# Kernel tuning notes

Hardware: AMD Instinct MI355X
Metric: run time of the kernel (lower is better)

## Reference

```python
import jax, jax.numpy as jnp
import numpy as np

E = 256  # embed_dim (hardcoded in source module)
H = 4    # n_head
D = E // H
SEQ = 32768


def setup_inputs() -> dict:
    key = jax.random.key(0)
    ks = jax.random.split(key, 5)
    x = jax.random.normal(ks[0], (SEQ, E), dtype=jnp.float32)
    in_proj_weight = jax.random.normal(ks[1], (3 * E, E), dtype=jnp.float32) * (1.0 / np.sqrt(E))
    in_proj_bias = jax.random.normal(ks[2], (3 * E,), dtype=jnp.float32) * 0.02
    out_proj_weight = jax.random.normal(ks[3], (E, E), dtype=jnp.float32) * (1.0 / np.sqrt(E))
    out_proj_bias = jax.random.normal(ks[4], (E,), dtype=jnp.float32) * 0.02
    return {
        "x": x,
        "in_proj_weight": in_proj_weight,
        "in_proj_bias": in_proj_bias,
        "out_proj_weight": out_proj_weight,
        "out_proj_bias": out_proj_bias,
    }


def reference(x, in_proj_weight, in_proj_bias, out_proj_weight, out_proj_bias):
    # QKV projections (q uses only the first token of x: single-query decode attention)
    Wq, Wk, Wv = in_proj_weight[:E], in_proj_weight[E:2 * E], in_proj_weight[2 * E:]
    bq, bk, bv = in_proj_bias[:E], in_proj_bias[E:2 * E], in_proj_bias[2 * E:]
    q = x[:1] @ Wq.T + bq            # [1, E]
    k = x @ Wk.T + bk                # [S, E]
    v = x @ Wv.T + bv                # [S, E]

    qh = q.reshape(H, D)             # [H, D] (single query)
    kh = k.reshape(-1, H, D)         # [S, H, D]
    vh = v.reshape(-1, H, D)         # [S, H, D]

    scale = 1.0 / np.sqrt(D).astype(np.float32)
    scores = jnp.einsum("hd,shd->hs", qh, kh) * scale   # [H, S]
    attn = jax.nn.softmax(scores, axis=-1)                # [H, S]
    ctx = jnp.einsum("hs,shd->hd", attn, vh)             # [H, D]

    out = ctx.reshape(1, E) @ out_proj_weight.T + out_proj_bias  # [1, E]
    return out
```

## Files before the change

kernel.cpp:

```cpp
#include <hip/hip_runtime.h>
#include <hip/hip_cooperative_groups.h>
namespace cg = cooperative_groups;

#define NBLK 256
#define WS_LP   0
#define WS_YV   1024
#define WS_B2   2048
#define WS_KQ   2304
#define WS_C4   3328
#define WS_M2   3392
#define WS_YP   265536

__device__ __forceinline__ float dot4(float4 a, float4 b) {
  return a.x * b.x + a.y * b.y + a.z * b.z + a.w * b.w;
}

__device__ __forceinline__ void phaseA_kq(const float* __restrict__ x, const float* __restrict__ W,
                                          const float* __restrict__ inb, float* __restrict__ kq,
                                          float* __restrict__ c4, float* sh, int bid, int t) {
  float* xs = sh;
  float* qls = sh + 256;
  float* red = sh + 320;
  const int lane = t & 63, w = t >> 6;
  const int h = bid >> 2, qt = bid & 3;
  if (t < 256) xs[t] = x[t];
  __syncthreads();
  const float4 xv = *(const float4*)&xs[lane * 4];
#pragma unroll
  for (int k = 0; k < 8; ++k) {
    const int eloc = w * 8 + k;
    const int row = h * 64 + eloc;
    float4 wv = *(const float4*)&W[(size_t)row * 256 + lane * 4];
    float p = dot4(wv, xv);
#pragma unroll
    for (int m = 1; m < 64; m <<= 1) p += __shfl_xor(p, m);
    if (lane == 0) qls[eloc] = p + inb[row];
  }
  __syncthreads();
  const int cl = t & 63, ds = t >> 6;
  float acc = 0.f;
#pragma unroll
  for (int d2 = 0; d2 < 8; ++d2) {
    const int d = ds * 8 + d2;
    acc += W[(size_t)(256 + h * 64 + d) * 256 + qt * 64 + cl] * qls[d];
  }
  red[ds * 64 + cl] = acc;
  __syncthreads();
  if (ds == 0) {
    float s = 0.f;
#pragma unroll
    for (int i = 0; i < 8; ++i) s += red[i * 64 + cl];
    kq[h * 256 + qt * 64 + cl] = s;
  }
  if (qt == 0 && t < 64) {
    float v = qls[t] * inb[256 + h * 64 + t];
#pragma unroll
    for (int m = 1; m < 64; m <<= 1) v += __shfl_xor(v, m);
    if (t == 0) c4[h] = v;
  }
}

__device__ __forceinline__ void phaseA_m2(const float* __restrict__ W, const float* __restrict__ Wout,
                                          float* __restrict__ M2, float* sh, int b2, int t) {
  float* wout_t = sh;
  const int tile = b2 >> 1, sub = b2 & 1;
  const int h = tile >> 4, e0 = (tile & 15) * 16 + sub * 8;
  {
    const int e = t >> 6, d = t & 63;
    wout_t[e * 64 + d] = Wout[(size_t)(e0 + e) * 256 + h * 64 + d];
  }
  __syncthreads();
  const int c = t & 255, eh = t >> 8;
  float acc[4] = {0.f, 0.f, 0.f, 0.f};
#pragma unroll 8
  for (int d = 0; d < 64; ++d) {
    const float wv = W[(size_t)(512 + h * 64 + d) * 256 + c];
#pragma unroll
    for (int e = 0; e < 4; ++e) acc[e] += wv * wout_t[(eh * 4 + e) * 64 + d];
  }
#pragma unroll
  for (int e = 0; e < 4; ++e)
    M2[(size_t)(e0 + eh * 4 + e) * 1024 + h * 256 + c] = acc[e];
}

__device__ __forceinline__ void phaseA_b2(const float* __restrict__ Wout, const float* __restrict__ inb,
                                          const float* __restrict__ bout, float* __restrict__ bias2,
                                          float* sh, int b, int t) {
  float* red = sh;
  const int og = t >> 5, seg = t & 31;
  const int e = b * 16 + og;
  float acc = 0.f;
#pragma unroll
  for (int j = 0; j < 8; ++j)
    acc += Wout[(size_t)e * 256 + seg * 8 + j] * inb[512 + seg * 8 + j];
  red[og * 32 + seg] = acc;
  __syncthreads();
  if (t < 16) {
    float s = bout[b * 16 + t];
#pragma unroll
    for (int i = 0; i < 32; ++i) s += red[t * 32 + i];
    bias2[b * 16 + t] = s;
  }
}

__device__ __forceinline__ float bscore(float4 xv, float4 kq0, float4 kq1, float4 kq2,
                                        float4 kq3, float c4v, int lane) {
  float p0 = dot4(xv, kq0), p1 = dot4(xv, kq1), p2 = dot4(xv, kq2), p3 = dot4(xv, kq3);
  const bool b1 = (lane & 2) != 0;
  float keep0 = b1 ? p2 : p0, send0 = b1 ? p0 : p2;
  keep0 += __shfl_xor(send0, 2);
  float keep1 = b1 ? p3 : p1, send1 = b1 ? p1 : p3;
  keep1 += __shfl_xor(send1, 2);
  const bool b0 = (lane & 1) != 0;
  float vv = b0 ? keep1 : keep0, sv = b0 ? keep0 : keep1;
  vv += __shfl_xor(sv, 1);
  vv += __shfl_xor(vv, 4);
  vv += __shfl_xor(vv, 8);
  vv += __shfl_xor(vv, 16);
  vv += __shfl_xor(vv, 32);
  return (vv + c4v) * 0.125f;
}

__device__ __forceinline__ void phaseB_core(const float4* xvA, const float4* xvB,
                                            const float* __restrict__ kq, const float* __restrict__ c4,
                                            float* __restrict__ ypart, float* __restrict__ lpart,
                                            float* yls, int bid, int t) {
  float* sll = yls + 8192;
  const int lane = t & 63, w = t >> 6;
  const int hme = lane & 3;
  const float4 kq0 = *(const float4*)&kq[0 * 256 + lane * 4];
  const float4 kq1 = *(const float4*)&kq[1 * 256 + lane * 4];
  const float4 kq2 = *(const float4*)&kq[2 * 256 + lane * 4];
  const float4 kq3 = *(const float4*)&kq[3 * 256 + lane * 4];
  const float c4v = c4[hme];

  float vA[8], vB[8];
#pragma unroll
  for (int r = 0; r < 8; ++r) vA[r] = bscore(xvA[r], kq0, kq1, kq2, kq3, c4v, lane);
#pragma unroll
  for (int r = 0; r < 8; ++r) vB[r] = bscore(xvB[r], kq0, kq1, kq2, kq3, c4v, lane);

  float l = 0.f;
  float4 a[4];
#pragma unroll
  for (int k = 0; k < 4; ++k) a[k] = (float4){0.f, 0.f, 0.f, 0.f};
#pragma unroll
  for (int r = 0; r < 8; ++r) {
    const float e0 = __expf(vA[r]);
    l += e0;
    const float e1 = __shfl_xor(e0, 1);
    const float e2 = __shfl_xor(e0, 2);
    const float e3 = __shfl_xor(e0, 3);
    a[0].x += e0 * xvA[r].x; a[0].y += e0 * xvA[r].y; a[0].z += e0 * xvA[r].z; a[0].w += e0 * xvA[r].w;
    a[1].x += e1 * xvA[r].x; a[1].y += e1 * xvA[r].y; a[1].z += e1 * xvA[r].z; a[1].w += e1 * xvA[r].w;
    a[2].x += e2 * xvA[r].x; a[2].y += e2 * xvA[r].y; a[2].z += e2 * xvA[r].z; a[2].w += e2 * xvA[r].w;
    a[3].x += e3 * xvA[r].x; a[3].y += e3 * xvA[r].y; a[3].z += e3 * xvA[r].z; a[3].w += e3 * xvA[r].w;
  }
#pragma unroll
  for (int r = 0; r < 8; ++r) {
    const float e0 = __expf(vB[r]);
    l += e0;
    const float e1 = __shfl_xor(e0, 1);
    const float e2 = __shfl_xor(e0, 2);
    const float e3 = __shfl_xor(e0, 3);
    a[0].x += e0 * xvB[r].x; a[0].y += e0 * xvB[r].y; a[0].z += e0 * xvB[r].z; a[0].w += e0 * xvB[r].w;
    a[1].x += e1 * xvB[r].x; a[1].y += e1 * xvB[r].y; a[1].z += e1 * xvB[r].z; a[1].w += e1 * xvB[r].w;
    a[2].x += e2 * xvB[r].x; a[2].y += e2 * xvB[r].y; a[2].z += e2 * xvB[r].z; a[2].w += e2 * xvB[r].w;
    a[3].x += e3 * xvB[r].x; a[3].y += e3 * xvB[r].y; a[3].z += e3 * xvB[r].z; a[3].w += e3 * xvB[r].w;
  }

  __syncthreads();
  if (lane < 4) sll[w * 4 + lane] = l;
#pragma unroll
  for (int k = 0; k < 4; ++k) {
    const int h = hme ^ k;
    *(float4*)&yls[w * 1024 + h * 256 + lane * 4] = a[k];
  }
  __syncthreads();

  if (t < 4) {
    float lb = 0.f;
#pragma unroll
    for (int i = 0; i < 8; ++i) lb += sll[i * 4 + t];
    lpart[t * NBLK + bid] = lb;
  }
  float* yp = &ypart[(size_t)bid * 1024];
#pragma unroll
  for (int o = t; o < 1024; o += 512) {
    float s = 0.f;
#pragma unroll
    for (int i = 0; i < 8; ++i) s += yls[i * 1024 + o];
    yp[o] = s;
  }
}

__device__ __forceinline__ void phaseC(const float* __restrict__ ypart, const float* __restrict__ lpart,
                                       float* __restrict__ z, float* sh, int bid, int t) {
  float* lred = sh;
  float* sred = sh + 256;
  const int h = bid >> 4;
  const int o0 = bid * 16;
  if (t < 256) lred[t] = lpart[h * 256 + t];
  __syncthreads();
  for (int s = 128; s > 0; s >>= 1) {
    if (t < s) lred[t] += lred[t + s];
    __syncthreads();
  }
  const float inv = 1.0f / lred[0];
  const int ol = t & 15, bg = t >> 4;
  float s = 0.f;
#pragma unroll
  for (int j = 0; j < 8; ++j) {
    const int b = bg * 8 + j;
    s += ypart[(size_t)b * 1024 + o0 + ol];
  }
  sred[bg * 16 + ol] = s;
  __syncthreads();
  if (t < 16) {
    float tot = 0.f;
#pragma unroll
    for (int g = 0; g < 32; ++g) tot += sred[g * 16 + t];
    z[o0 + t] = tot * inv;
  }
}

__device__ __forceinline__ void phaseD(const float* __restrict__ M2, const float* __restrict__ z,
                                       const float* __restrict__ bias2, float* __restrict__ out,
                                       float* sh, int bid, int t) {
  float* zls = sh;
  float* smo = sh + 1024;
  for (int i = t; i < 1024; i += 512) zls[i] = z[i];
  __syncthreads();
  const int og = t >> 5, seg = t & 31;
  const int e = bid * 16 + og;
  float acc = 0.f;
  const float4* m4 = (const float4*)&M2[(size_t)e * 1024 + seg * 32];
  const float4* z4 = (const float4*)&zls[seg * 32];
#pragma unroll
  for (int j = 0; j < 8; ++j) acc += dot4(m4[j], z4[j]);
  smo[og * 32 + seg] = acc;
  __syncthreads();
  if (t < 16) {
    float s = bias2[bid * 16 + t];
#pragma unroll
    for (int i = 0; i < 32; ++i) s += smo[t * 32 + i];
    out[bid * 16 + t] = s;
  }
}

__global__ void __launch_bounds__(512, 1) mha_coop(const float* __restrict__ x,
                                                   const float* __restrict__ W,
                                                   const float* __restrict__ inb,
                                                   const float* __restrict__ Wout,
                                                   const float* __restrict__ bout,
                                                   float* __restrict__ out,
                                                   float* __restrict__ ws) {
  __shared__ __align__(16) float sh[8224];
  const int t = threadIdx.x, bid = blockIdx.x;
  const int lane = t & 63, w = t >> 6;
  cg::grid_group grid = cg::this_grid();

  const int r0 = bid * 128 + w * 16;
  float4 xvA[8], xvB[8];

  if (bid >= 16) {
#pragma unroll
    for (int r = 0; r < 8; ++r)
      xvA[r] = *(const float4*)&x[(size_t)(r0 + r) * 256 + lane * 4];
#pragma unroll
    for (int r = 0; r < 8; ++r)
      xvB[r] = *(const float4*)&x[(size_t)(r0 + 8 + r) * 256 + lane * 4];
  }

  if (bid < 16) {
    phaseA_kq(x, W, inb, ws + WS_KQ, ws + WS_C4, sh, bid, t);
#pragma unroll
    for (int r = 0; r < 8; ++r)
      xvA[r] = *(const float4*)&x[(size_t)(r0 + r) * 256 + lane * 4];
#pragma unroll
    for (int r = 0; r < 8; ++r)
      xvB[r] = *(const float4*)&x[(size_t)(r0 + 8 + r) * 256 + lane * 4];
  } else if (bid < 144) {
    phaseA_m2(W, Wout, ws + WS_M2, sh, bid - 16, t);
  } else if (bid < 160) {
    phaseA_b2(Wout, inb, bout, ws + WS_B2, sh, bid - 144, t);
  }

  grid.sync();
  phaseB_core(xvA, xvB, ws + WS_KQ, ws + WS_C4, ws + WS_YP, ws + WS_LP, sh, bid, t);
  grid.sync();
  if (bid < 64) phaseC(ws + WS_YP, ws + WS_LP, ws + WS_YV, sh, bid, t);
  grid.sync();
  if (bid < 16) phaseD(ws + WS_M2, ws + WS_YV, ws + WS_B2, out, sh, bid, t);
}

__global__ void __launch_bounds__(512) fb_A(const float* __restrict__ x, const float* __restrict__ W,
                                            const float* __restrict__ inb, const float* __restrict__ Wout,
                                            const float* __restrict__ bout, float* __restrict__ ws) {
  __shared__ __align__(16) float sh[832];
  const int bid = blockIdx.x, t = threadIdx.x;
  if (bid < 16) phaseA_kq(x, W, inb, ws + WS_KQ, ws + WS_C4, sh, bid, t);
  else if (bid < 144) phaseA_m2(W, Wout, ws + WS_M2, sh, bid - 16, t);
  else if (bid < 160) phaseA_b2(Wout, inb, bout, ws + WS_B2, sh, bid - 144, t);
}
__global__ void __launch_bounds__(512) fb_B(const float* __restrict__ x, float* __restrict__ ws) {
  __shared__ __align__(16) float sh[8224];
  const int bid = blockIdx.x, t = threadIdx.x;
  const int lane = t & 63, w = t >> 6;
  const int r0 = bid * 128 + w * 16;
  float4 xvA[8], xvB[8];
#pragma unroll
  for (int r = 0; r < 8; ++r)
    xvA[r] = *(const float4*)&x[(size_t)(r0 + r) * 256 + lane * 4];
#pragma unroll
  for (int r = 0; r < 8; ++r)
    xvB[r] = *(const float4*)&x[(size_t)(r0 + 8 + r) * 256 + lane * 4];
  phaseB_core(xvA, xvB, ws + WS_KQ, ws + WS_C4, ws + WS_YP, ws + WS_LP, sh, bid, t);
}
__global__ void __launch_bounds__(512) fb_C(float* __restrict__ ws) {
  __shared__ __align__(16) float sh[768];
  phaseC(ws + WS_YP, ws + WS_LP, ws + WS_YV, sh, blockIdx.x, threadIdx.x);
}
__global__ void __launch_bounds__(512) fb_D(float* __restrict__ out, float* __restrict__ ws) {
  __shared__ __align__(16) float sh[1536];
  phaseD(ws + WS_M2, ws + WS_YV, ws + WS_B2, out, sh, blockIdx.x, threadIdx.x);
}

extern "C" void kernel_launch(void* const* d_in, const int* in_sizes, int n_in,
                              void* d_out, int out_size, void* d_ws, size_t ws_size,
                              hipStream_t stream) {
  const float* x = (const float*)d_in[0];
  const float* W = (const float*)d_in[1];
  const float* inb = (const float*)d_in[2];
  const float* Wout = (const float*)d_in[3];
  const float* bout = (const float*)d_in[4];
  float* out = (float*)d_out;
  float* ws = (float*)d_ws;

  int dev = 0;
  (void)hipGetDevice(&dev);
  int coopAttr = 0, ncu = 0, occ = 0;
  bool coop = (hipDeviceGetAttribute(&coopAttr, hipDeviceAttributeCooperativeLaunch, dev) == hipSuccess) &&
              coopAttr != 0;
  coop = coop &&
         (hipDeviceGetAttribute(&ncu, hipDeviceAttributeMultiprocessorCount, dev) == hipSuccess);
  coop = coop &&
         (hipOccupancyMaxActiveBlocksPerMultiprocessor(&occ, mha_coop, 512, 0) == hipSuccess);
  coop = coop && (occ * ncu >= NBLK);

  if (coop) {
    void* args[] = {(void*)&x, (void*)&W, (void*)&inb, (void*)&Wout,
                    (void*)&bout, (void*)&out, (void*)&ws};
    if (hipLaunchCooperativeKernel((const void*)mha_coop, dim3(NBLK), dim3(512),
                                   args, 0, stream) == hipSuccess)
      return;
  }
  fb_A<<<160, 512, 0, stream>>>(x, W, inb, Wout, bout, ws);
  fb_B<<<NBLK, 512, 0, stream>>>(x, ws);
  fb_C<<<64, 512, 0, stream>>>(ws);
  fb_D<<<16, 512, 0, stream>>>(out, ws);
}
```

Before: 31.87 us.

## Project per-block context through Wv in phase B and drop M2 precompute

Removes the precomputed M2 = Wv^T·Wout fusion and bias2 blocks. Each phase-B block now multiplies its partial x-weighted sums by Wv to produce a 256-wide per-block context partial. A single final phase reduces the partials, normalises by the softmax sums, adds the value bias and applies the output projection. This removes one grid-wide sync and the large M2 matrix write and read, at the cost of every block reading the full 256x256 Wv slice.

```diff
diff --git a/kernel.cpp b/kernel.cpp
--- a/kernel.cpp
+++ b/kernel.cpp
@@ -4,12 +4,9 @@
 
 #define NBLK 256
 #define WS_LP   0
-#define WS_YV   1024
-#define WS_B2   2048
-#define WS_KQ   2304
-#define WS_C4   3328
-#define WS_M2   3392
-#define WS_YP   265536
+#define WS_KQ   1024
+#define WS_C4   2048
+#define WS_CTXP 2112
 
 __device__ __forceinline__ float dot4(float4 a, float4 b) {
   return a.x * b.x + a.y * b.y + a.z * b.z + a.w * b.w;
@@ -57,49 +54,6 @@
 #pragma unroll
     for (int m = 1; m < 64; m <<= 1) v += __shfl_xor(v, m);
     if (t == 0) c4[h] = v;
-  }
-}
-
-__device__ __forceinline__ void phaseA_m2(const float* __restrict__ W, const float* __restrict__ Wout,
-                                          float* __restrict__ M2, float* sh, int b2, int t) {
-  float* wout_t = sh;
-  const int tile = b2 >> 1, sub = b2 & 1;
-  const int h = tile >> 4, e0 = (tile & 15) * 16 + sub * 8;
-  {
-    const int e = t >> 6, d = t & 63;
-    wout_t[e * 64 + d] = Wout[(size_t)(e0 + e) * 256 + h * 64 + d];
-  }
-  __syncthreads();
-  const int c = t & 255, eh = t >> 8;
-  float acc[4] = {0.f, 0.f, 0.f, 0.f};
-#pragma unroll 8
-  for (int d = 0; d < 64; ++d) {
-    const float wv = W[(size_t)(512 + h * 64 + d) * 256 + c];
-#pragma unroll
-    for (int e = 0; e < 4; ++e) acc[e] += wv * wout_t[(eh * 4 + e) * 64 + d];
-  }
-#pragma unroll
-  for (int e = 0; e < 4; ++e)
-    M2[(size_t)(e0 + eh * 4 + e) * 1024 + h * 256 + c] = acc[e];
-}
-
-__device__ __forceinline__ void phaseA_b2(const float* __restrict__ Wout, const float* __restrict__ inb,
-                                          const float* __restrict__ bout, float* __restrict__ bias2,
-                                          float* sh, int b, int t) {
-  float* red = sh;
-  const int og = t >> 5, seg = t & 31;
-  const int e = b * 16 + og;
-  float acc = 0.f;
-#pragma unroll
-  for (int j = 0; j < 8; ++j)
-    acc += Wout[(size_t)e * 256 + seg * 8 + j] * inb[512 + seg * 8 + j];
-  red[og * 32 + seg] = acc;
-  __syncthreads();
-  if (t < 16) {
-    float s = bout[b * 16 + t];
-#pragma unroll
-    for (int i = 0; i < 32; ++i) s += red[t * 32 + i];
-    bias2[b * 16 + t] = s;
   }
 }
 
@@ -123,7 +77,8 @@
 
 __device__ __forceinline__ void phaseB_core(const float4* xvA, const float4* xvB,
                                             const float* __restrict__ kq, const float* __restrict__ c4,
-                                            float* __restrict__ ypart, float* __restrict__ lpart,
+                                            const float* __restrict__ W,
+                                            float* __restrict__ lpart, float* __restrict__ ctxp,
                                             float* yls, int bid, int t) {
   float* sll = yls + 8192;
   const int lane = t & 63, w = t >> 6;
@@ -184,67 +139,73 @@
     for (int i = 0; i < 8; ++i) lb += sll[i * 4 + t];
     lpart[t * NBLK + bid] = lb;
   }
-  float* yp = &ypart[(size_t)bid * 1024];
 #pragma unroll
   for (int o = t; o < 1024; o += 512) {
     float s = 0.f;
 #pragma unroll
     for (int i = 0; i < 8; ++i) s += yls[i * 1024 + o];
-    yp[o] = s;
-  }
-}
-
-__device__ __forceinline__ void phaseC(const float* __restrict__ ypart, const float* __restrict__ lpart,
-                                       float* __restrict__ z, float* sh, int bid, int t) {
-  float* lred = sh;
-  float* sred = sh + 256;
-  const int h = bid >> 4;
-  const int o0 = bid * 16;
-  if (t < 256) lred[t] = lpart[h * 256 + t];
-  __syncthreads();
-  for (int s = 128; s > 0; s >>= 1) {
-    if (t < s) lred[t] += lred[t + s];
-    __syncthreads();
-  }
-  const float inv = 1.0f / lred[0];
-  const int ol = t & 15, bg = t >> 4;
-  float s = 0.f;
-#pragma unroll
-  for (int j = 0; j < 8; ++j) {
-    const int b = bg * 8 + j;
-    s += ypart[(size_t)b * 1024 + o0 + ol];
-  }
-  sred[bg * 16 + ol] = s;
-  __syncthreads();
-  if (t < 16) {
-    float tot = 0.f;
-#pragma unroll
-    for (int g = 0; g < 32; ++g) tot += sred[g * 16 + t];
-    z[o0 + t] = tot * inv;
-  }
-}
-
-__device__ __forceinline__ void phaseD(const float* __restrict__ M2, const float* __restrict__ z,
-                                       const float* __restrict__ bias2, float* __restrict__ out,
+    yls[o] = s;
+  }
+  __syncthreads();
+
+  float* co = &ctxp[(size_t)bid * 256];
+  for (int k = 0; k < 32; k += 4) {
+    float p[4];
+#pragma unroll
+    for (int j = 0; j < 4; ++j) {
+      const int ii = w * 32 + k + j;
+      float4 wv = *(const float4*)&W[(size_t)(512 + ii) * 256 + lane * 4];
+      float4 yy = *(const float4*)&yls[(ii >> 6) * 256 + lane * 4];
+      p[j] = dot4(wv, yy);
+    }
+#pragma unroll
+    for (int m = 1; m < 64; m <<= 1) {
+#pragma unroll
+      for (int j = 0; j < 4; ++j) p[j] += __shfl_xor(p[j], m);
+    }
+    if (lane == 0) {
+#pragma unroll
+      for (int j = 0; j < 4; ++j) co[w * 32 + k + j] = p[j];
+    }
+  }
+}
+
+__device__ __forceinline__ void phaseF(const float* __restrict__ inb, const float* __restrict__ Wout,
+                                       const float* __restrict__ bout, const float* __restrict__ lpart,
+                                       const float* __restrict__ ctxp, float* __restrict__ out,
                                        float* sh, int bid, int t) {
-  float* zls = sh;
-  float* smo = sh + 1024;
-  for (int i = t; i < 1024; i += 512) zls[i] = z[i];
-  __syncthreads();
-  const int og = t >> 5, seg = t & 31;
-  const int e = bid * 16 + og;
-  float acc = 0.f;
-  const float4* m4 = (const float4*)&M2[(size_t)e * 1024 + seg * 32];
-  const float4* z4 = (const float4*)&zls[seg * 32];
-#pragma unroll
-  for (int j = 0; j < 8; ++j) acc += dot4(m4[j], z4[j]);
-  smo[og * 32 + seg] = acc;
-  __syncthreads();
-  if (t < 16) {
-    float s = bias2[bid * 16 + t];
-#pragma unroll
-    for (int i = 0; i < 32; ++i) s += smo[t * 32 + i];
-    out[bid * 16 + t] = s;
+  float* linv = sh;
+  float* sctx = sh + 16;
+  float* ctxls = sh + 528;
+  const int lane = t & 63, w = t >> 6;
+  if (w < 4) {
+    float s = 0.f;
+#pragma unroll
+    for (int j = 0; j < 4; ++j) s += lpart[w * 256 + j * 64 + lane];
+#pragma unroll
+    for (int m = 1; m < 64; m <<= 1) s += __shfl_xor(s, m);
+    if (lane == 0) linv[w] = 1.0f / s;
+  }
+  const int i = t & 255, part = t >> 8;
+  {
+    float s = 0.f;
+    const float* cp = ctxp + (size_t)part * 128 * 256 + i;
+#pragma unroll 8
+    for (int b = 0; b < 128; ++b) s += cp[(size_t)b * 256];
+    sctx[part * 256 + i] = s;
+  }
+  __syncthreads();
+  if (t < 256) ctxls[t] = (sctx[t] + sctx[256 + t]) * linv[t >> 6] + inb[512 + t];
+  __syncthreads();
+  const float4 cv = *(const float4*)&ctxls[lane * 4];
+#pragma unroll
+  for (int k = 0; k < 2; ++k) {
+    const int e = bid * 16 + w * 2 + k;
+    float4 wv = *(const float4*)&Wout[(size_t)e * 256 + lane * 4];
+    float p = dot4(wv, cv);
+#pragma unroll
+    for (int m = 1; m < 64; m <<= 1) p += __shfl_xor(p, m);
+    if (lane == 0) out[e] = p + bout[e];
   }
 }
 
@@ -280,30 +241,21 @@
 #pragma unroll
     for (int r = 0; r < 8; ++r)
       xvB[r] = *(const float4*)&x[(size_t)(r0 + 8 + r) * 256 + lane * 4];
-  } else if (bid < 144) {
-    phaseA_m2(W, Wout, ws + WS_M2, sh, bid - 16, t);
-  } else if (bid < 160) {
-    phaseA_b2(Wout, inb, bout, ws + WS_B2, sh, bid - 144, t);
   }
 
   grid.sync();
-  phaseB_core(xvA, xvB, ws + WS_KQ, ws + WS_C4, ws + WS_YP, ws + WS_LP, sh, bid, t);
+  phaseB_core(xvA, xvB, ws + WS_KQ, ws + WS_C4, W, ws + WS_LP, ws + WS_CTXP, sh, bid, t);
   grid.sync();
-  if (bid < 64) phaseC(ws + WS_YP, ws + WS_LP, ws + WS_YV, sh, bid, t);
-  grid.sync();
-  if (bid < 16) phaseD(ws + WS_M2, ws + WS_YV, ws + WS_B2, out, sh, bid, t);
+  if (bid < 16) phaseF(inb, Wout, bout, ws + WS_LP, ws + WS_CTXP, out, sh, bid, t);
 }
 
 __global__ void __launch_bounds__(512) fb_A(const float* __restrict__ x, const float* __restrict__ W,
-                                            const float* __restrict__ inb, const float* __restrict__ Wout,
-                                            const float* __restrict__ bout, float* __restrict__ ws) {
+                                            const float* __restrict__ inb, float* __restrict__ ws) {
   __shared__ __align__(16) float sh[832];
-  const int bid = blockIdx.x, t = threadIdx.x;
-  if (bid < 16) phaseA_kq(x, W, inb, ws + WS_KQ, ws + WS_C4, sh, bid, t);
-  else if (bid < 144) phaseA_m2(W, Wout, ws + WS_M2, sh, bid - 16, t);
-  else if (bid < 160) phaseA_b2(Wout, inb, bout, ws + WS_B2, sh, bid - 144, t);
-}
-__global__ void __launch_bounds__(512) fb_B(const float* __restrict__ x, float* __restrict__ ws) {
+  phaseA_kq(x, W, inb, ws + WS_KQ, ws + WS_C4, sh, blockIdx.x, threadIdx.x);
+}
+__global__ void __launch_bounds__(512) fb_B(const float* __restrict__ x, const float* __restrict__ W,
+                                            float* __restrict__ ws) {
   __shared__ __align__(16) float sh[8224];
   const int bid = blockIdx.x, t = threadIdx.x;
   const int lane = t & 63, w = t >> 6;
@@ -315,15 +267,13 @@
 #pragma unroll
   for (int r = 0; r < 8; ++r)
     xvB[r] = *(const float4*)&x[(size_t)(r0 + 8 + r) * 256 + lane * 4];
-  phaseB_core(xvA, xvB, ws + WS_KQ, ws + WS_C4, ws + WS_YP, ws + WS_LP, sh, bid, t);
-}
-__global__ void __launch_bounds__(512) fb_C(float* __restrict__ ws) {
-  __shared__ __align__(16) float sh[768];
-  phaseC(ws + WS_YP, ws + WS_LP, ws + WS_YV, sh, blockIdx.x, threadIdx.x);
-}
-__global__ void __launch_bounds__(512) fb_D(float* __restrict__ out, float* __restrict__ ws) {
-  __shared__ __align__(16) float sh[1536];
-  phaseD(ws + WS_M2, ws + WS_YV, ws + WS_B2, out, sh, blockIdx.x, threadIdx.x);
+  phaseB_core(xvA, xvB, ws + WS_KQ, ws + WS_C4, W, ws + WS_LP, ws + WS_CTXP, sh, bid, t);
+}
+__global__ void __launch_bounds__(512) fb_F(const float* __restrict__ inb, const float* __restrict__ Wout,
+                                            const float* __restrict__ bout, float* __restrict__ out,
+                                            float* __restrict__ ws) {
+  __shared__ __align__(16) float sh[800];
+  phaseF(inb, Wout, bout, ws + WS_LP, ws + WS_CTXP, out, sh, blockIdx.x, threadIdx.x);
 }
 
 extern "C" void kernel_launch(void* const* d_in, const int* in_sizes, int n_in,
@@ -355,8 +305,7 @@
                                    args, 0, stream) == hipSuccess)
       return;
   }
-  fb_A<<<160, 512, 0, stream>>>(x, W, inb, Wout, bout, ws);
-  fb_B<<<NBLK, 512, 0, stream>>>(x, ws);
-  fb_C<<<64, 512, 0, stream>>>(ws);
-  fb_D<<<16, 512, 0, stream>>>(out, ws);
-}
+  fb_A<<<16, 512, 0, stream>>>(x, W, inb, ws);
+  fb_B<<<NBLK, 512, 0, stream>>>(x, W, ws);
+  fb_F<<<16, 512, 0, stream>>>(inb, Wout, bout, out, ws);
+}
```

Result: slower. 38.47 us (+20.7%).

## Replace grid syncs with flag polling and fuse final phases via atomic ticket

Applied to the files above, without the earlier changes.

Replaces the first grid-wide barrier with per-block release flags that phase B polls, so blocks only wait for the 16 kq-producing blocks rather than the whole grid. Merges the normalization and output-projection phases into a single 16-block phase whose partial sums go into a fixed-point integer buffer through atomics, with the last block (chosen by an atomic ticket) writing the output. This drops two grid syncs, at the cost of spin-polling, fixed-point quantization of the output accumulation, and workspace that must be reset on every call.

```diff
diff --git a/kernel.cpp b/kernel.cpp
--- a/kernel.cpp
+++ b/kernel.cpp
@@ -3,16 +3,37 @@
 namespace cg = cooperative_groups;
 
 #define NBLK 256
+#define MAGIC 0x5A5A5A5A
+#define SCALE 4194304.0f
+#define INV_SCALE 2.38418579e-7f
+
 #define WS_LP   0
-#define WS_YV   1024
-#define WS_B2   2048
-#define WS_KQ   2304
-#define WS_C4   3328
-#define WS_M2   3392
-#define WS_YP   265536
+#define WS_KQ   1024
+#define WS_C4   2048
+#define WS_B2   2112
+#define WS_M2   2368
+#define WS_YP   264512
+#define WS_ACC  526656
+#define WS_TK   530752
+#define WS_FLA  530768
 
 __device__ __forceinline__ float dot4(float4 a, float4 b) {
   return a.x * b.x + a.y * b.y + a.z * b.z + a.w * b.w;
+}
+
+__device__ __forceinline__ void set_flag(int* slot, int t) {
+  __threadfence();
+  __syncthreads();
+  if (t == 0) __hip_atomic_store(slot, MAGIC, __ATOMIC_RELEASE, __HIP_MEMORY_SCOPE_AGENT);
+}
+__device__ __forceinline__ void poll_flags(const int* flags, int n, int t) {
+  const int idx = t & (n - 1);
+  for (;;) {
+    int v = __hip_atomic_load((int*)&flags[idx], __ATOMIC_RELAXED, __HIP_MEMORY_SCOPE_AGENT);
+    if (__syncthreads_and(v == MAGIC)) break;
+    __builtin_amdgcn_s_sleep(2);
+  }
+  __threadfence();
 }
 
 __device__ __forceinline__ void phaseA_kq(const float* __restrict__ x, const float* __restrict__ W,
@@ -194,57 +215,59 @@
   }
 }
 
-__device__ __forceinline__ void phaseC(const float* __restrict__ ypart, const float* __restrict__ lpart,
-                                       float* __restrict__ z, float* sh, int bid, int t) {
-  float* lred = sh;
-  float* sred = sh + 256;
-  const int h = bid >> 4;
-  const int o0 = bid * 16;
-  if (t < 256) lred[t] = lpart[h * 256 + t];
-  __syncthreads();
-  for (int s = 128; s > 0; s >>= 1) {
-    if (t < s) lred[t] += lred[t + s];
-    __syncthreads();
-  }
-  const float inv = 1.0f / lred[0];
-  const int ol = t & 15, bg = t >> 4;
-  float s = 0.f;
-#pragma unroll
-  for (int j = 0; j < 8; ++j) {
-    const int b = bg * 8 + j;
-    s += ypart[(size_t)b * 1024 + o0 + ol];
-  }
-  sred[bg * 16 + ol] = s;
-  __syncthreads();
-  if (t < 16) {
+__device__ __forceinline__ void phaseCF(const float* __restrict__ lpart, const float* __restrict__ ypart,
+                                        const float* __restrict__ M2, const float* __restrict__ bias2,
+                                        float* __restrict__ out, int* __restrict__ out_acc,
+                                        int* __restrict__ ticket, float* sh, int bid, int t) {
+  float* z = sh;
+  float* zred = sh + 64;
+  float* linv = sh + 576;
+  __shared__ int tk;
+  const int lane = t & 63, w = t >> 6;
+  const int h = bid >> 2;
+  const int base = bid * 64;
+  if (w == 0) {
+    float s = 0.f;
+#pragma unroll
+    for (int j = 0; j < 4; ++j) s += lpart[h * 256 + j * 64 + lane];
+#pragma unroll
+    for (int m = 1; m < 64; m <<= 1) s += __shfl_xor(s, m);
+    if (lane == 0) linv[0] = 1.0f / s;
+  }
+  const int i = t >> 3, g = t & 7;
+  {
+    float s = 0.f;
+#pragma unroll 8
+    for (int j = 0; j < 32; ++j) {
+      const int b = g * 32 + j;
+      s += ypart[(size_t)b * 1024 + base + i];
+    }
+    zred[i * 8 + g] = s;
+  }
+  __syncthreads();
+  if (t < 64) {
     float tot = 0.f;
 #pragma unroll
-    for (int g = 0; g < 32; ++g) tot += sred[g * 16 + t];
-    z[o0 + t] = tot * inv;
-  }
-}
-
-__device__ __forceinline__ void phaseD(const float* __restrict__ M2, const float* __restrict__ z,
-                                       const float* __restrict__ bias2, float* __restrict__ out,
-                                       float* sh, int bid, int t) {
-  float* zls = sh;
-  float* smo = sh + 1024;
-  for (int i = t; i < 1024; i += 512) zls[i] = z[i];
-  __syncthreads();
-  const int og = t >> 5, seg = t & 31;
-  const int e = bid * 16 + og;
+    for (int gg = 0; gg < 8; ++gg) tot += zred[t * 8 + gg];
+    z[t] = tot * linv[0];
+  }
+  __syncthreads();
+  const int e = t >> 1, half = t & 1;
+  const float4* m4 = (const float4*)&M2[(size_t)e * 1024 + base + half * 32];
+  const float4* z4 = (const float4*)&z[half * 32];
   float acc = 0.f;
-  const float4* m4 = (const float4*)&M2[(size_t)e * 1024 + seg * 32];
-  const float4* z4 = (const float4*)&zls[seg * 32];
 #pragma unroll
   for (int j = 0; j < 8; ++j) acc += dot4(m4[j], z4[j]);
-  smo[og * 32 + seg] = acc;
-  __syncthreads();
-  if (t < 16) {
-    float s = bias2[bid * 16 + t];
-#pragma unroll
-    for (int i = 0; i < 32; ++i) s += smo[t * 32 + i];
-    out[bid * 16 + t] = s;
+  acc += __shfl_xor(acc, 1);
+  if (half == 0) atomicAdd(&out_acc[e * 16], __float2int_rn(acc * SCALE));
+  __threadfence();
+  __syncthreads();
+  if (t == 0)
+    tk = __hip_atomic_fetch_add(ticket, 1, __ATOMIC_ACQ_REL, __HIP_MEMORY_SCOPE_AGENT);
+  __syncthreads();
+  if (tk == 15 && t < 256) {
+    int v = __hip_atomic_load(&out_acc[t * 16], __ATOMIC_RELAXED, __HIP_MEMORY_SCOPE_AGENT);
+    out[t] = (float)v * INV_SCALE + bias2[t];
   }
 }
 
@@ -258,6 +281,9 @@
   __shared__ __align__(16) float sh[8224];
   const int t = threadIdx.x, bid = blockIdx.x;
   const int lane = t & 63, w = t >> 6;
+  int* flagA = (int*)(ws + WS_FLA);
+  int* out_acc = (int*)(ws + WS_ACC);
+  int* ticket = (int*)(ws + WS_TK);
   cg::grid_group grid = cg::this_grid();
 
   const int r0 = bid * 128 + w * 16;
@@ -274,6 +300,7 @@
 
   if (bid < 16) {
     phaseA_kq(x, W, inb, ws + WS_KQ, ws + WS_C4, sh, bid, t);
+    set_flag(&flagA[bid], t);
 #pragma unroll
     for (int r = 0; r < 8; ++r)
       xvA[r] = *(const float4*)&x[(size_t)(r0 + r) * 256 + lane * 4];
@@ -284,14 +311,19 @@
     phaseA_m2(W, Wout, ws + WS_M2, sh, bid - 16, t);
   } else if (bid < 160) {
     phaseA_b2(Wout, inb, bout, ws + WS_B2, sh, bid - 144, t);
-  }
+  } else if (bid == 200) {
+    for (int j = t; j < 4096; j += 512) out_acc[j] = 0;
+    if (t == 0) *ticket = 0;
+  }
+
+  poll_flags(flagA, 16, t);
+  phaseB_core(xvA, xvB, ws + WS_KQ, ws + WS_C4, ws + WS_YP, ws + WS_LP, sh, bid, t);
 
   grid.sync();
-  phaseB_core(xvA, xvB, ws + WS_KQ, ws + WS_C4, ws + WS_YP, ws + WS_LP, sh, bid, t);
-  grid.sync();
-  if (bid < 64) phaseC(ws + WS_YP, ws + WS_LP, ws + WS_YV, sh, bid, t);
-  grid.sync();
-  if (bid < 16) phaseD(ws + WS_M2, ws + WS_YV, ws + WS_B2, out, sh, bid, t);
+
+  if (bid == 16 && t < 16) flagA[t] = 0;
+  if (bid < 16)
+    phaseCF(ws + WS_LP, ws + WS_YP, ws + WS_M2, ws + WS_B2, out, out_acc, ticket, sh, bid, t);
 }
 
 __global__ void __launch_bounds__(512) fb_A(const float* __restrict__ x, const float* __restrict__ W,
@@ -302,6 +334,11 @@
   if (bid < 16) phaseA_kq(x, W, inb, ws + WS_KQ, ws + WS_C4, sh, bid, t);
   else if (bid < 144) phaseA_m2(W, Wout, ws + WS_M2, sh, bid - 16, t);
   else if (bid < 160) phaseA_b2(Wout, inb, bout, ws + WS_B2, sh, bid - 144, t);
+  else {
+    int* out_acc = (int*)(ws + WS_ACC);
+    for (int j = t; j < 4096; j += 512) out_acc[j] = 0;
+    if (t == 0) *(int*)(ws + WS_TK) = 0;
+  }
 }
 __global__ void __launch_bounds__(512) fb_B(const float* __restrict__ x, float* __restrict__ ws) {
   __shared__ __align__(16) float sh[8224];
@@ -317,13 +354,10 @@
     xvB[r] = *(const float4*)&x[(size_t)(r0 + 8 + r) * 256 + lane * 4];
   phaseB_core(xvA, xvB, ws + WS_KQ, ws + WS_C4, ws + WS_YP, ws + WS_LP, sh, bid, t);
 }
-__global__ void __launch_bounds__(512) fb_C(float* __restrict__ ws) {
-  __shared__ __align__(16) float sh[768];
-  phaseC(ws + WS_YP, ws + WS_LP, ws + WS_YV, sh, blockIdx.x, threadIdx.x);
-}
-__global__ void __launch_bounds__(512) fb_D(float* __restrict__ out, float* __restrict__ ws) {
-  __shared__ __align__(16) float sh[1536];
-  phaseD(ws + WS_M2, ws + WS_YV, ws + WS_B2, out, sh, blockIdx.x, threadIdx.x);
+__global__ void __launch_bounds__(512) fb_CF(float* __restrict__ out, float* __restrict__ ws) {
+  __shared__ __align__(16) float sh[600];
+  phaseCF(ws + WS_LP, ws + WS_YP, ws + WS_M2, ws + WS_B2, out,
+          (int*)(ws + WS_ACC), (int*)(ws + WS_TK), sh, blockIdx.x, threadIdx.x);
 }
 
 extern "C" void kernel_launch(void* const* d_in, const int* in_sizes, int n_in,
@@ -355,8 +389,7 @@
                                    args, 0, stream) == hipSuccess)
       return;
   }
-  fb_A<<<160, 512, 0, stream>>>(x, W, inb, Wout, bout, ws);
+  fb_A<<<161, 512, 0, stream>>>(x, W, inb, Wout, bout, ws);
   fb_B<<<NBLK, 512, 0, stream>>>(x, ws);
-  fb_C<<<64, 512, 0, stream>>>(ws);
-  fb_D<<<16, 512, 0, stream>>>(out, ws);
-}
+  fb_CF<<<16, 512, 0, stream>>>(out, ws);
+}
```

After: 34.34 us. +7.7%, slower.

## Move weight-only precompute after attention phase and give kq its own blocks

Applied to the files above, without the earlier changes.

The cooperative grid grows from 256 to 272 blocks. Sixteen extra blocks compute the query/key-projection vectors while the 256 attention blocks only prefetch their x rows, which shortens the work before the first grid sync. The weight-only M2 and bias precompute moves out of that first phase and runs alongside the phase-C reduction, off the critical path. This needs two blocks per CU (launch bounds raised to 2), which may limit registers for the register-heavy phaseB. If the occupancy check fails, the code falls back to the slower multi-kernel path.

```diff
diff --git a/kernel.cpp b/kernel.cpp
--- a/kernel.cpp
+++ b/kernel.cpp
@@ -2,7 +2,8 @@
 #include <hip/hip_cooperative_groups.h>
 namespace cg = cooperative_groups;
 
-#define NBLK 256
+#define NBLK 272
+#define NB_B 256
 #define WS_LP   0
 #define WS_YV   1024
 #define WS_B2   2048
@@ -17,12 +18,12 @@
 
 __device__ __forceinline__ void phaseA_kq(const float* __restrict__ x, const float* __restrict__ W,
                                           const float* __restrict__ inb, float* __restrict__ kq,
-                                          float* __restrict__ c4, float* sh, int bid, int t) {
+                                          float* __restrict__ c4, float* sh, int ab, int t) {
   float* xs = sh;
   float* qls = sh + 256;
   float* red = sh + 320;
   const int lane = t & 63, w = t >> 6;
-  const int h = bid >> 2, qt = bid & 3;
+  const int h = ab >> 2, qt = ab & 3;
   if (t < 256) xs[t] = x[t];
   __syncthreads();
   const float4 xv = *(const float4*)&xs[lane * 4];
@@ -182,7 +183,7 @@
     float lb = 0.f;
 #pragma unroll
     for (int i = 0; i < 8; ++i) lb += sll[i * 4 + t];
-    lpart[t * NBLK + bid] = lb;
+    lpart[t * NB_B + bid] = lb;
   }
   float* yp = &ypart[(size_t)bid * 1024];
 #pragma unroll
@@ -248,7 +249,7 @@
   }
 }
 
-__global__ void __launch_bounds__(512, 1) mha_coop(const float* __restrict__ x,
+__global__ void __launch_bounds__(512, 2) mha_coop(const float* __restrict__ x,
                                                    const float* __restrict__ W,
                                                    const float* __restrict__ inb,
                                                    const float* __restrict__ Wout,
@@ -260,48 +261,35 @@
   const int lane = t & 63, w = t >> 6;
   cg::grid_group grid = cg::this_grid();
 
-  const int r0 = bid * 128 + w * 16;
   float4 xvA[8], xvB[8];
 
-  if (bid >= 16) {
+  if (bid < NB_B) {
+    const int r0 = bid * 128 + w * 16;
 #pragma unroll
     for (int r = 0; r < 8; ++r)
       xvA[r] = *(const float4*)&x[(size_t)(r0 + r) * 256 + lane * 4];
 #pragma unroll
     for (int r = 0; r < 8; ++r)
       xvB[r] = *(const float4*)&x[(size_t)(r0 + 8 + r) * 256 + lane * 4];
-  }
-
-  if (bid < 16) {
-    phaseA_kq(x, W, inb, ws + WS_KQ, ws + WS_C4, sh, bid, t);
-#pragma unroll
-    for (int r = 0; r < 8; ++r)
-      xvA[r] = *(const float4*)&x[(size_t)(r0 + r) * 256 + lane * 4];
-#pragma unroll
-    for (int r = 0; r < 8; ++r)
-      xvB[r] = *(const float4*)&x[(size_t)(r0 + 8 + r) * 256 + lane * 4];
-  } else if (bid < 144) {
-    phaseA_m2(W, Wout, ws + WS_M2, sh, bid - 16, t);
-  } else if (bid < 160) {
-    phaseA_b2(Wout, inb, bout, ws + WS_B2, sh, bid - 144, t);
+  } else {
+    phaseA_kq(x, W, inb, ws + WS_KQ, ws + WS_C4, sh, bid - NB_B, t);
   }
 
   grid.sync();
-  phaseB_core(xvA, xvB, ws + WS_KQ, ws + WS_C4, ws + WS_YP, ws + WS_LP, sh, bid, t);
+  if (bid < NB_B)
+    phaseB_core(xvA, xvB, ws + WS_KQ, ws + WS_C4, ws + WS_YP, ws + WS_LP, sh, bid, t);
   grid.sync();
   if (bid < 64) phaseC(ws + WS_YP, ws + WS_LP, ws + WS_YV, sh, bid, t);
+  else if (bid < 192) phaseA_m2(W, Wout, ws + WS_M2, sh, bid - 64, t);
+  else if (bid < 208) phaseA_b2(Wout, inb, bout, ws + WS_B2, sh, bid - 192, t);
   grid.sync();
   if (bid < 16) phaseD(ws + WS_M2, ws + WS_YV, ws + WS_B2, out, sh, bid, t);
 }
 
 __global__ void __launch_bounds__(512) fb_A(const float* __restrict__ x, const float* __restrict__ W,
-                                            const float* __restrict__ inb, const float* __restrict__ Wout,
-                                            const float* __restrict__ bout, float* __restrict__ ws) {
+                                            const float* __restrict__ inb, float* __restrict__ ws) {
   __shared__ __align__(16) float sh[832];
-  const int bid = blockIdx.x, t = threadIdx.x;
-  if (bid < 16) phaseA_kq(x, W, inb, ws + WS_KQ, ws + WS_C4, sh, bid, t);
-  else if (bid < 144) phaseA_m2(W, Wout, ws + WS_M2, sh, bid - 16, t);
-  else if (bid < 160) phaseA_b2(Wout, inb, bout, ws + WS_B2, sh, bid - 144, t);
+  phaseA_kq(x, W, inb, ws + WS_KQ, ws + WS_C4, sh, blockIdx.x, threadIdx.x);
 }
 __global__ void __launch_bounds__(512) fb_B(const float* __restrict__ x, float* __restrict__ ws) {
   __shared__ __align__(16) float sh[8224];
@@ -317,9 +305,14 @@
     xvB[r] = *(const float4*)&x[(size_t)(r0 + 8 + r) * 256 + lane * 4];
   phaseB_core(xvA, xvB, ws + WS_KQ, ws + WS_C4, ws + WS_YP, ws + WS_LP, sh, bid, t);
 }
-__global__ void __launch_bounds__(512) fb_C(float* __restrict__ ws) {
-  __shared__ __align__(16) float sh[768];
-  phaseC(ws + WS_YP, ws + WS_LP, ws + WS_YV, sh, blockIdx.x, threadIdx.x);
+__global__ void __launch_bounds__(512) fb_CM(const float* __restrict__ W, const float* __restrict__ Wout,
+                                             const float* __restrict__ inb, const float* __restrict__ bout,
+                                             float* __restrict__ ws) {
+  __shared__ __align__(16) float sh[832];
+  const int bid = blockIdx.x, t = threadIdx.x;
+  if (bid < 64) phaseC(ws + WS_YP, ws + WS_LP, ws + WS_YV, sh, bid, t);
+  else if (bid < 192) phaseA_m2(W, Wout, ws + WS_M2, sh, bid - 64, t);
+  else if (bid < 208) phaseA_b2(Wout, inb, bout, ws + WS_B2, sh, bid - 192, t);
 }
 __global__ void __launch_bounds__(512) fb_D(float* __restrict__ out, float* __restrict__ ws) {
   __shared__ __align__(16) float sh[1536];
@@ -355,8 +348,8 @@
                                    args, 0, stream) == hipSuccess)
       return;
   }
-  fb_A<<<160, 512, 0, stream>>>(x, W, inb, Wout, bout, ws);
-  fb_B<<<NBLK, 512, 0, stream>>>(x, ws);
-  fb_C<<<64, 512, 0, stream>>>(ws);
+  fb_A<<<16, 512, 0, stream>>>(x, W, inb, ws);
+  fb_B<<<NB_B, 512, 0, stream>>>(x, ws);
+  fb_CM<<<208, 512, 0, stream>>>(W, Wout, inb, bout, ws);
   fb_D<<<16, 512, 0, stream>>>(out, ws);
 }
```

Result: slower. 33.87 us (+6.3%).
